# Kernel optimization log

Measured on AMD Instinct MI355X. Metric: run time of the kernel, lower is better.

Reference implementation:

```python
import jax, jax.numpy as jnp
import numpy as np

NEG_INF = -1e9  # stand-in for -inf so fully-masked rows stay finite


def setup_inputs() -> dict:
    key = jax.random.key(0)
    ks = jax.random.split(key, 7)
    B, Nq, Nkv, H, D = 8, 512, 512, 16, 256
    return {
        "v_inv": jax.random.normal(ks[0], (B, Nkv, D), dtype=jnp.float32),
        "messages": jax.random.normal(ks[1], (B, Nq, Nkv, H), dtype=jnp.float32),
        "adj_matrix": jax.random.randint(ks[2], (B, Nq, Nkv), 0, 2, dtype=jnp.int32),
        "W_in": jax.random.normal(ks[3], (D, D), dtype=jnp.float32) * (1.0 / np.sqrt(D)),
        "b_in": jax.random.normal(ks[4], (D,), dtype=jnp.float32) * 0.02,
        "W_out": jax.random.normal(ks[5], (D, D), dtype=jnp.float32) * (1.0 / np.sqrt(D)),
        "b_out": jax.random.normal(ks[6], (D,), dtype=jnp.float32) * 0.02,
    }


def reference(v_inv, messages, adj_matrix, W_in, b_in, W_out, b_out):
    H = messages.shape[-1]
    D = v_inv.shape[-1]
    d_head = D // H
    # adjacency -> additive attention mask (0 where edge, -inf where not)
    attn_mask = jnp.where(adj_matrix > 0, 0.0, NEG_INF).astype(messages.dtype)
    logits = messages + attn_mask[..., None]          # [B, Nq, Nkv, H]
    attn = jax.nn.softmax(logits, axis=2)             # softmax over N_kv
    # value projection and head split
    proj = v_inv @ W_in.T + b_in                      # [B, Nkv, D]
    head_feats = proj.reshape(*proj.shape[:-1], H, d_head)  # [B, Nkv, H, dh]
    # per-head weighted aggregation of value features
    attn_out = jnp.einsum("bqkh,bkhd->bqhd", attn, head_feats)  # [B, Nq, H, dh]
    # L2 norm of attention row per head, used as a rescale
    weights = jnp.sqrt(jnp.sum(attn * attn, axis=2))  # [B, Nq, H]
    attn_out = attn_out * weights[..., None]
    attn_out = attn_out.reshape(*attn_out.shape[:-2], D)  # [B, Nq, D]
    return attn_out @ W_out.T + b_out
```

## Files before the change

### kernel.cpp

```cpp
#include <hip/hip_runtime.h>

constexpr int NQ = 512;
constexpr int NKV = 512;
constexpr int Hh = 16;
constexpr int Dd = 256;

__global__ __launch_bounds__(256) void gemm_bias(
    const float* __restrict__ A, const float* __restrict__ W,
    const float* __restrict__ bias, float* __restrict__ C) {
  __shared__ float As[64][68];
  __shared__ float Ws[64][68];
  const int t = threadIdx.x;
  const int tx = t & 15, ty = t >> 4;
  const int m0 = blockIdx.x * 64, n0 = blockIdx.y * 64;

  float acc[4][4] = {};
  float4 av[4], wv[4];

#pragma unroll
  for (int i = 0; i < 4; ++i) {
    const int flat = i * 256 + t;
    const int r = flat >> 4, c4 = (flat & 15) << 2;
    av[i] = *(const float4*)(A + (size_t)(m0 + r) * 256 + c4);
    wv[i] = *(const float4*)(W + (size_t)(n0 + r) * 256 + c4);
  }

  for (int kb = 0; kb < 4; ++kb) {
#pragma unroll
    for (int i = 0; i < 4; ++i) {
      const int flat = i * 256 + t;
      const int r = flat >> 4, c4 = (flat & 15) << 2;
      As[c4 + 0][r] = av[i].x; As[c4 + 1][r] = av[i].y;
      As[c4 + 2][r] = av[i].z; As[c4 + 3][r] = av[i].w;
      Ws[c4 + 0][r] = wv[i].x; Ws[c4 + 1][r] = wv[i].y;
      Ws[c4 + 2][r] = wv[i].z; Ws[c4 + 3][r] = wv[i].w;
    }
    __syncthreads();
    if (kb < 3) {
#pragma unroll
      for (int i = 0; i < 4; ++i) {
        const int flat = i * 256 + t;
        const int r = flat >> 4, c4 = (flat & 15) << 2;
        av[i] = *(const float4*)(A + (size_t)(m0 + r) * 256 + (kb + 1) * 64 + c4);
        wv[i] = *(const float4*)(W + (size_t)(n0 + r) * 256 + (kb + 1) * 64 + c4);
      }
    }
#pragma unroll 16
    for (int k = 0; k < 64; ++k) {
      float a_[4], w_[4];
      *(float4*)a_ = *(const float4*)&As[k][ty << 2];
      *(float4*)w_ = *(const float4*)&Ws[k][tx << 2];
#pragma unroll
      for (int i = 0; i < 4; ++i)
#pragma unroll
        for (int j = 0; j < 4; ++j)
          acc[i][j] = fmaf(a_[i], w_[j], acc[i][j]);
    }
    if (kb < 3) __syncthreads();
  }

  const float4 bv = *(const float4*)(bias + n0 + (tx << 2));
  const float bb[4] = {bv.x, bv.y, bv.z, bv.w};
#pragma unroll
  for (int i = 0; i < 4; ++i) {
    float4 cv;
    cv.x = acc[i][0] + bb[0]; cv.y = acc[i][1] + bb[1];
    cv.z = acc[i][2] + bb[2]; cv.w = acc[i][3] + bb[3];
    *(float4*)(C + (size_t)(m0 + (ty << 2) + i) * 256 + n0 + (tx << 2)) = cv;
  }
}

__global__ __launch_bounds__(512, 4) void attn_fused(
    const float* __restrict__ msg, const int* __restrict__ adj,
    const float* __restrict__ proj, float* __restrict__ attn_out) {
  __shared__ float Psh[4][8][256];
  __shared__ float Esh[4][8][16][12];

  const int t    = threadIdx.x;
  const int lane = t & 63;
  const int w    = t >> 6;
  const int oct  = w >> 1;
  const int qh   = w & 1;
  const int h    = lane >> 2;
  const int d4   = lane & 3;
  const int col  = lane << 2;
  const int q0   = blockIdx.x * 8;
  const int b    = blockIdx.y;

  const int p_h4  = t & 3;
  const int p_q   = (t >> 2) & 7;
  const int p_oct = (t >> 5) & 3;
  const int p_jp  = t >> 7;

  const float* mrow = msg + ((size_t)(b * NQ + q0 + p_q) * NKV) * Hh + p_h4 * 4;
  const int*   arow = adj + (size_t)(b * NQ + q0 + p_q) * NKV;
  const float* pb   = proj + (size_t)b * NKV * Dd;

  float4 o[4] = {};
  float s[4] = {}, r[4] = {};

  float4 mv0, mv1;
  int a0, a1;
  {
    const int kg = p_oct * 128 + p_jp * 2;
    mv0 = *(const float4*)(mrow + (size_t)kg * Hh);
    mv1 = *(const float4*)(mrow + (size_t)(kg + 1) * Hh);
    a0 = arow[kg]; a1 = arow[kg + 1];
  }

  for (int rd = 0; rd < 16; ++rd) {
#pragma unroll
    for (int i = 0; i < 4; ++i) {
      const float* g = pb + (size_t)(i * 128 + rd * 8 + w) * Dd + (lane << 2);
      __builtin_amdgcn_global_load_lds(
          (const __attribute__((address_space(1))) unsigned int*)g,
          (__attribute__((address_space(3))) unsigned int*)&Psh[i][w][0],
          16, 0, 0);
    }
    {
      float e0[4], e1[4];
      e0[0] = a0 > 0 ? __expf(mv0.x) : 0.f; e0[1] = a0 > 0 ? __expf(mv0.y) : 0.f;
      e0[2] = a0 > 0 ? __expf(mv0.z) : 0.f; e0[3] = a0 > 0 ? __expf(mv0.w) : 0.f;
      e1[0] = a1 > 0 ? __expf(mv1.x) : 0.f; e1[1] = a1 > 0 ? __expf(mv1.y) : 0.f;
      e1[2] = a1 > 0 ? __expf(mv1.z) : 0.f; e1[3] = a1 > 0 ? __expf(mv1.w) : 0.f;
#pragma unroll
      for (int i = 0; i < 4; ++i) {
        const int h2 = (p_h4 * 4 + i) ^ p_q;
        *(float2*)&Esh[p_oct][p_q][h2][p_jp * 2] = make_float2(e0[i], e1[i]);
      }
    }
    __syncthreads();

    if (rd < 15) {
      const int kg = p_oct * 128 + (rd + 1) * 8 + p_jp * 2;
      mv0 = *(const float4*)(mrow + (size_t)kg * Hh);
      mv1 = *(const float4*)(mrow + (size_t)(kg + 1) * Hh);
      a0 = arow[kg]; a1 = arow[kg + 1];
    }

    __builtin_amdgcn_s_setprio(1);
#pragma unroll
    for (int kh = 0; kh < 2; ++kh) {
      float4 p[4];
#pragma unroll
      for (int j = 0; j < 4; ++j)
        p[j] = *(const float4*)&Psh[oct][kh * 4 + j][col];
#pragma unroll
      for (int qi = 0; qi < 4; ++qi) {
        const int ql = qh * 4 + qi;
        const float4 e4 = *(const float4*)&Esh[oct][ql][h ^ ql][kh * 4];
        s[qi] += e4.x + e4.y + e4.z + e4.w;
        r[qi] = fmaf(e4.x, e4.x, fmaf(e4.y, e4.y,
                fmaf(e4.z, e4.z, fmaf(e4.w, e4.w, r[qi]))));
        o[qi].x = fmaf(e4.x, p[0].x, o[qi].x);
        o[qi].y = fmaf(e4.x, p[0].y, o[qi].y);
        o[qi].z = fmaf(e4.x, p[0].z, o[qi].z);
        o[qi].w = fmaf(e4.x, p[0].w, o[qi].w);
        o[qi].x = fmaf(e4.y, p[1].x, o[qi].x);
        o[qi].y = fmaf(e4.y, p[1].y, o[qi].y);
        o[qi].z = fmaf(e4.y, p[1].z, o[qi].z);
        o[qi].w = fmaf(e4.y, p[1].w, o[qi].w);
        o[qi].x = fmaf(e4.z, p[2].x, o[qi].x);
        o[qi].y = fmaf(e4.z, p[2].y, o[qi].y);
        o[qi].z = fmaf(e4.z, p[2].z, o[qi].z);
        o[qi].w = fmaf(e4.z, p[2].w, o[qi].w);
        o[qi].x = fmaf(e4.w, p[3].x, o[qi].x);
        o[qi].y = fmaf(e4.w, p[3].y, o[qi].y);
        o[qi].z = fmaf(e4.w, p[3].z, o[qi].z);
        o[qi].w = fmaf(e4.w, p[3].w, o[qi].w);
      }
    }
    __builtin_amdgcn_s_setprio(0);
    if (rd < 15) __syncthreads();
  }

  float4* Ro = (float4*)&Psh[0][0][0];
  float*  Rs = &Esh[0][0][0][0];
  float*  Rr = Rs + 256;

  __syncthreads();
  if (w >= 4) {
    const int reg = w - 4;
#pragma unroll
    for (int qi = 0; qi < 4; ++qi) {
      Ro[(reg * 4 + qi) * 64 + lane] = o[qi];
      if (d4 == 0) {
        Rs[(reg * 4 + qi) * 16 + h] = s[qi];
        Rr[(reg * 4 + qi) * 16 + h] = r[qi];
      }
    }
  }
  __syncthreads();
  if (w < 4) {
#pragma unroll
    for (int qi = 0; qi < 4; ++qi) {
      const float4 v = Ro[(w * 4 + qi) * 64 + lane];
      o[qi].x += v.x; o[qi].y += v.y; o[qi].z += v.z; o[qi].w += v.w;
      s[qi] += Rs[(w * 4 + qi) * 16 + h];
      r[qi] += Rr[(w * 4 + qi) * 16 + h];
    }
  }
  __syncthreads();
  if (w == 2 || w == 3) {
    const int reg = w - 2;
#pragma unroll
    for (int qi = 0; qi < 4; ++qi) {
      Ro[(reg * 4 + qi) * 64 + lane] = o[qi];
      if (d4 == 0) {
        Rs[(reg * 4 + qi) * 16 + h] = s[qi];
        Rr[(reg * 4 + qi) * 16 + h] = r[qi];
      }
    }
  }
  __syncthreads();
  if (w < 2) {
#pragma unroll
    for (int qi = 0; qi < 4; ++qi) {
      const float4 v = Ro[(w * 4 + qi) * 64 + lane];
      o[qi].x += v.x; o[qi].y += v.y; o[qi].z += v.z; o[qi].w += v.w;
      const float st = s[qi] + Rs[(w * 4 + qi) * 16 + h];
      const float rt = r[qi] + Rr[(w * 4 + qi) * 16 + h];
      const float wgt = sqrtf(rt) / (st * st);
      float4 u;
      u.x = o[qi].x * wgt; u.y = o[qi].y * wgt;
      u.z = o[qi].z * wgt; u.w = o[qi].w * wgt;
      const int q = q0 + w * 4 + qi;
      *(float4*)(attn_out + (size_t)(b * NQ + q) * Dd + col) = u;
    }
  }
}

extern "C" void kernel_launch(void* const* d_in, const int* in_sizes, int n_in,
                              void* d_out, int out_size, void* d_ws, size_t ws_size,
                              hipStream_t stream) {
  const float* v_inv    = (const float*)d_in[0];
  const float* messages = (const float*)d_in[1];
  const int*   adj      = (const int*)d_in[2];
  const float* W_in     = (const float*)d_in[3];
  const float* b_in     = (const float*)d_in[4];
  const float* W_out    = (const float*)d_in[5];
  const float* b_out    = (const float*)d_in[6];
  float* out = (float*)d_out;

  float* proj = (float*)d_ws;
  float* attn = proj + (size_t)8 * NKV * Dd;

  dim3 gg(64, 4);
  gemm_bias<<<gg, 256, 0, stream>>>(v_inv, W_in, b_in, proj);
  attn_fused<<<dim3(64, 8), 512, 0, stream>>>(messages, adj, proj, attn);
  gemm_bias<<<gg, 256, 0, stream>>>(attn, W_out, b_out, out);
}
```

Before: 251.1 us.

## Load proj rows directly to registers and double-buffer exp tile with single barrier

Each wave now reads its eight proj rows straight from global memory into registers instead of staging them through shared memory with global_load_lds. The exp-weight tile in LDS is double-buffered, so each round needs only one barrier instead of two. The loop is unrolled by two with ping-pong message/adjacency prefetch registers, and the adjacency pair is loaded as one int2. This cuts LDS traffic and synchronisation, but adds register pressure and redundant global/L2 reads of proj, since both waves per octant now load the same rows.

```diff
diff --git a/kernel.cpp b/kernel.cpp
--- a/kernel.cpp
+++ b/kernel.cpp
@@ -73,8 +73,7 @@
 __global__ __launch_bounds__(512, 4) void attn_fused(
     const float* __restrict__ msg, const int* __restrict__ adj,
     const float* __restrict__ proj, float* __restrict__ attn_out) {
-  __shared__ float Psh[4][8][256];
-  __shared__ float Esh[4][8][16][12];
+  __shared__ float Esh[2][4][8][16][12];
 
   const int t    = threadIdx.x;
   const int lane = t & 63;
@@ -99,84 +98,90 @@
   float4 o[4] = {};
   float s[4] = {}, r[4] = {};
 
-  float4 mv0, mv1;
-  int a0, a1;
+  float4 mA0, mA1, mB0, mB1;
+  int2 aA, aB;
   {
     const int kg = p_oct * 128 + p_jp * 2;
-    mv0 = *(const float4*)(mrow + (size_t)kg * Hh);
-    mv1 = *(const float4*)(mrow + (size_t)(kg + 1) * Hh);
-    a0 = arow[kg]; a1 = arow[kg + 1];
-  }
-
-  for (int rd = 0; rd < 16; ++rd) {
-#pragma unroll
-    for (int i = 0; i < 4; ++i) {
-      const float* g = pb + (size_t)(i * 128 + rd * 8 + w) * Dd + (lane << 2);
-      __builtin_amdgcn_global_load_lds(
-          (const __attribute__((address_space(1))) unsigned int*)g,
-          (__attribute__((address_space(3))) unsigned int*)&Psh[i][w][0],
-          16, 0, 0);
-    }
-    {
-      float e0[4], e1[4];
-      e0[0] = a0 > 0 ? __expf(mv0.x) : 0.f; e0[1] = a0 > 0 ? __expf(mv0.y) : 0.f;
-      e0[2] = a0 > 0 ? __expf(mv0.z) : 0.f; e0[3] = a0 > 0 ? __expf(mv0.w) : 0.f;
-      e1[0] = a1 > 0 ? __expf(mv1.x) : 0.f; e1[1] = a1 > 0 ? __expf(mv1.y) : 0.f;
-      e1[2] = a1 > 0 ? __expf(mv1.z) : 0.f; e1[3] = a1 > 0 ? __expf(mv1.w) : 0.f;
-#pragma unroll
-      for (int i = 0; i < 4; ++i) {
-        const int h2 = (p_h4 * 4 + i) ^ p_q;
-        *(float2*)&Esh[p_oct][p_q][h2][p_jp * 2] = make_float2(e0[i], e1[i]);
-      }
-    }
-    __syncthreads();
-
-    if (rd < 15) {
-      const int kg = p_oct * 128 + (rd + 1) * 8 + p_jp * 2;
-      mv0 = *(const float4*)(mrow + (size_t)kg * Hh);
-      mv1 = *(const float4*)(mrow + (size_t)(kg + 1) * Hh);
-      a0 = arow[kg]; a1 = arow[kg + 1];
-    }
-
-    __builtin_amdgcn_s_setprio(1);
-#pragma unroll
-    for (int kh = 0; kh < 2; ++kh) {
-      float4 p[4];
-#pragma unroll
-      for (int j = 0; j < 4; ++j)
-        p[j] = *(const float4*)&Psh[oct][kh * 4 + j][col];
-#pragma unroll
-      for (int qi = 0; qi < 4; ++qi) {
-        const int ql = qh * 4 + qi;
-        const float4 e4 = *(const float4*)&Esh[oct][ql][h ^ ql][kh * 4];
-        s[qi] += e4.x + e4.y + e4.z + e4.w;
-        r[qi] = fmaf(e4.x, e4.x, fmaf(e4.y, e4.y,
-                fmaf(e4.z, e4.z, fmaf(e4.w, e4.w, r[qi]))));
-        o[qi].x = fmaf(e4.x, p[0].x, o[qi].x);
-        o[qi].y = fmaf(e4.x, p[0].y, o[qi].y);
-        o[qi].z = fmaf(e4.x, p[0].z, o[qi].z);
-        o[qi].w = fmaf(e4.x, p[0].w, o[qi].w);
-        o[qi].x = fmaf(e4.y, p[1].x, o[qi].x);
-        o[qi].y = fmaf(e4.y, p[1].y, o[qi].y);
-        o[qi].z = fmaf(e4.y, p[1].z, o[qi].z);
-        o[qi].w = fmaf(e4.y, p[1].w, o[qi].w);
-        o[qi].x = fmaf(e4.z, p[2].x, o[qi].x);
-        o[qi].y = fmaf(e4.z, p[2].y, o[qi].y);
-        o[qi].z = fmaf(e4.z, p[2].z, o[qi].z);
-        o[qi].w = fmaf(e4.z, p[2].w, o[qi].w);
-        o[qi].x = fmaf(e4.w, p[3].x, o[qi].x);
-        o[qi].y = fmaf(e4.w, p[3].y, o[qi].y);
-        o[qi].z = fmaf(e4.w, p[3].z, o[qi].z);
-        o[qi].w = fmaf(e4.w, p[3].w, o[qi].w);
-      }
-    }
-    __builtin_amdgcn_s_setprio(0);
-    if (rd < 15) __syncthreads();
-  }
-
-  float4* Ro = (float4*)&Psh[0][0][0];
-  float*  Rs = &Esh[0][0][0][0];
-  float*  Rr = Rs + 256;
+    mA0 = *(const float4*)(mrow + (size_t)kg * Hh);
+    mA1 = *(const float4*)(mrow + (size_t)(kg + 1) * Hh);
+    aA = *(const int2*)(arow + kg);
+  }
+
+#define ATTN_ROUND(RD, BUF, MC0, MC1, AC, MN0, MN1, AN)                        \
+  {                                                                            \
+     \
+     \
+    float4 p4[8];                                                              \
+    _Pragma("unroll")                                                          \
+    for (int j = 0; j < 8; ++j)                                                \
+      p4[j] = *(const float4*)(pb + (size_t)(oct * 128 + (RD) * 8 + j) * Dd + col); \
+    {                                                                          \
+      float e0[4], e1[4];                                                      \
+      e0[0] = AC.x > 0 ? __expf(MC0.x) : 0.f;                                  \
+      e0[1] = AC.x > 0 ? __expf(MC0.y) : 0.f;                                  \
+      e0[2] = AC.x > 0 ? __expf(MC0.z) : 0.f;                                  \
+      e0[3] = AC.x > 0 ? __expf(MC0.w) : 0.f;                                  \
+      e1[0] = AC.y > 0 ? __expf(MC1.x) : 0.f;                                  \
+      e1[1] = AC.y > 0 ? __expf(MC1.y) : 0.f;                                  \
+      e1[2] = AC.y > 0 ? __expf(MC1.z) : 0.f;                                  \
+      e1[3] = AC.y > 0 ? __expf(MC1.w) : 0.f;                                  \
+      _Pragma("unroll")                                                        \
+      for (int i = 0; i < 4; ++i) {                                            \
+        const int h2 = (p_h4 * 4 + i) ^ p_q;                                   \
+        *(float2*)&Esh[BUF][p_oct][p_q][h2][p_jp * 2] =                        \
+            make_float2(e0[i], e1[i]);                                         \
+      }                                                                        \
+    }                                                                          \
+    if ((RD) < 15) {  \
+      const int kg = p_oct * 128 + ((RD) + 1) * 8 + p_jp * 2;                  \
+      MN0 = *(const float4*)(mrow + (size_t)kg * Hh);                          \
+      MN1 = *(const float4*)(mrow + (size_t)(kg + 1) * Hh);                    \
+      AN = *(const int2*)(arow + kg);                                          \
+    }                                                                          \
+    asm volatile("s_waitcnt lgkmcnt(0)" ::: "memory");   \
+    __builtin_amdgcn_s_barrier();                                              \
+    __builtin_amdgcn_s_setprio(1);                                             \
+    _Pragma("unroll")                                                          \
+    for (int kh = 0; kh < 2; ++kh) {                                           \
+      _Pragma("unroll")                                                        \
+      for (int qi = 0; qi < 4; ++qi) {                                         \
+        const int ql = qh * 4 + qi;                                            \
+        const float4 e4 = *(const float4*)&Esh[BUF][oct][ql][h ^ ql][kh * 4];  \
+        s[qi] += e4.x + e4.y + e4.z + e4.w;                                    \
+        r[qi] = fmaf(e4.x, e4.x, fmaf(e4.y, e4.y,                              \
+                fmaf(e4.z, e4.z, fmaf(e4.w, e4.w, r[qi]))));                   \
+        o[qi].x = fmaf(e4.x, p4[kh * 4 + 0].x, o[qi].x);                       \
+        o[qi].y = fmaf(e4.x, p4[kh * 4 + 0].y, o[qi].y);                       \
+        o[qi].z = fmaf(e4.x, p4[kh * 4 + 0].z, o[qi].z);                       \
+        o[qi].w = fmaf(e4.x, p4[kh * 4 + 0].w, o[qi].w);                       \
+        o[qi].x = fmaf(e4.y, p4[kh * 4 + 1].x, o[qi].x);                       \
+        o[qi].y = fmaf(e4.y, p4[kh * 4 + 1].y, o[qi].y);                       \
+        o[qi].z = fmaf(e4.y, p4[kh * 4 + 1].z, o[qi].z);                       \
+        o[qi].w = fmaf(e4.y, p4[kh * 4 + 1].w, o[qi].w);                       \
+        o[qi].x = fmaf(e4.z, p4[kh * 4 + 2].x, o[qi].x);                       \
+        o[qi].y = fmaf(e4.z, p4[kh * 4 + 2].y, o[qi].y);                       \
+        o[qi].z = fmaf(e4.z, p4[kh * 4 + 2].z, o[qi].z);                       \
+        o[qi].w = fmaf(e4.z, p4[kh * 4 + 2].w, o[qi].w);                       \
+        o[qi].x = fmaf(e4.w, p4[kh * 4 + 3].x, o[qi].x);                       \
+        o[qi].y = fmaf(e4.w, p4[kh * 4 + 3].y, o[qi].y);                       \
+        o[qi].z = fmaf(e4.w, p4[kh * 4 + 3].z, o[qi].z);                       \
+        o[qi].w = fmaf(e4.w, p4[kh * 4 + 3].w, o[qi].w);                       \
+      }                                                                        \
+    }                                                                          \
+    __builtin_amdgcn_s_setprio(0);                                             \
+  }
+
+  for (int rr = 0; rr < 8; ++rr) {
+    const int rdE = rr * 2;
+    ATTN_ROUND(rdE,     0, mA0, mA1, aA, mB0, mB1, aB);
+    ATTN_ROUND(rdE + 1, 1, mB0, mB1, aB, mA0, mA1, aA);
+  }
+#undef ATTN_ROUND
+
+  float*  base = &Esh[0][0][0][0][0];
+  float4* Ro = (float4*)base;
+  float*  Rs = base + 4096;
+  float*  Rr = base + 4352;
 
   __syncthreads();
   if (w >= 4) {
```

After: 419.3 us. 67.0% more time.

## Double-buffer attention LDS stages with smaller k-chunks and one barrier per round

Applied to the files above, without the earlier changes.

Restructures the attention kernel main loop to use double-buffered shared memory for the projected values and exponentiated logits. The k-chunk per round drops from 8 to 4 keys, so there are now 32 rounds. The next chunk's global-to-LDS loads and message loads are issued before computing on the current buffer, and the exp/mask write goes to the alternate buffer after compute, leaving one barrier per round instead of two. This aims to hide global load latency behind FMA work, at the cost of more loop iterations with less compute each.

```diff
diff --git a/kernel.cpp b/kernel.cpp
--- a/kernel.cpp
+++ b/kernel.cpp
@@ -73,8 +73,8 @@
 __global__ __launch_bounds__(512, 4) void attn_fused(
     const float* __restrict__ msg, const int* __restrict__ adj,
     const float* __restrict__ proj, float* __restrict__ attn_out) {
-  __shared__ float Psh[4][8][256];
-  __shared__ float Esh[4][8][16][12];
+  __shared__ float Psh[2][4][4][256];
+  __shared__ float Esh[2][4][8][16][4];
 
   const int t    = threadIdx.x;
   const int lane = t & 63;
@@ -90,92 +90,122 @@
   const int p_h4  = t & 3;
   const int p_q   = (t >> 2) & 7;
   const int p_oct = (t >> 5) & 3;
-  const int p_jp  = t >> 7;
-
-  const float* mrow = msg + ((size_t)(b * NQ + q0 + p_q) * NKV) * Hh + p_h4 * 4;
-  const int*   arow = adj + (size_t)(b * NQ + q0 + p_q) * NKV;
-  const float* pb   = proj + (size_t)b * NKV * Dd;
+  const int p_kk  = t >> 7;
+
+  const int sa = w * 2, sb = w * 2 + 1;
+  const int sa_oct = sa >> 2, sa_kk = sa & 3;
+  const int sb_oct = sb >> 2, sb_kk = sb & 3;
+
+  const float* mrow  = msg + ((size_t)(b * NQ + q0 + p_q) * NKV) * Hh + p_h4 * 4;
+  const int*   arow  = adj + (size_t)(b * NQ + q0 + p_q) * NKV;
+  const float* pbase = proj + (size_t)b * NKV * Dd;
 
   float4 o[4] = {};
   float s[4] = {}, r[4] = {};
 
-  float4 mv0, mv1;
-  int a0, a1;
+  float4 mv; int aa;
+
   {
-    const int kg = p_oct * 128 + p_jp * 2;
-    mv0 = *(const float4*)(mrow + (size_t)kg * Hh);
-    mv1 = *(const float4*)(mrow + (size_t)(kg + 1) * Hh);
-    a0 = arow[kg]; a1 = arow[kg + 1];
-  }
-
-  for (int rd = 0; rd < 16; ++rd) {
-#pragma unroll
-    for (int i = 0; i < 4; ++i) {
-      const float* g = pb + (size_t)(i * 128 + rd * 8 + w) * Dd + (lane << 2);
+    const int kg = p_oct * 128 + p_kk;
+    mv = *(const float4*)(mrow + (size_t)kg * Hh);
+    aa = arow[kg];
+    const float* ga = pbase + (size_t)(sa_oct * 128 + sa_kk) * Dd + (lane << 2);
+    __builtin_amdgcn_global_load_lds(
+        (const __attribute__((address_space(1))) unsigned int*)ga,
+        (__attribute__((address_space(3))) unsigned int*)&Psh[0][sa_oct][sa_kk][0],
+        16, 0, 0);
+    const float* gb = pbase + (size_t)(sb_oct * 128 + sb_kk) * Dd + (lane << 2);
+    __builtin_amdgcn_global_load_lds(
+        (const __attribute__((address_space(1))) unsigned int*)gb,
+        (__attribute__((address_space(3))) unsigned int*)&Psh[0][sb_oct][sb_kk][0],
+        16, 0, 0);
+    float e[4];
+    e[0] = aa > 0 ? __expf(mv.x) : 0.f;
+    e[1] = aa > 0 ? __expf(mv.y) : 0.f;
+    e[2] = aa > 0 ? __expf(mv.z) : 0.f;
+    e[3] = aa > 0 ? __expf(mv.w) : 0.f;
+#pragma unroll
+    for (int i = 0; i < 4; ++i)
+      Esh[0][p_oct][p_q][(p_h4 * 4 + i) ^ p_q][p_kk] = e[i];
+  }
+  __syncthreads();
+
+#pragma unroll 1
+  for (int rd = 0; rd < 32; ++rd) {
+    const int cur = rd & 1, nxt = cur ^ 1;
+    if (rd < 31) {
+      const float* ga =
+          pbase + (size_t)(sa_oct * 128 + (rd + 1) * 4 + sa_kk) * Dd + (lane << 2);
       __builtin_amdgcn_global_load_lds(
-          (const __attribute__((address_space(1))) unsigned int*)g,
-          (__attribute__((address_space(3))) unsigned int*)&Psh[i][w][0],
+          (const __attribute__((address_space(1))) unsigned int*)ga,
+          (__attribute__((address_space(3))) unsigned int*)&Psh[nxt][sa_oct][sa_kk][0],
           16, 0, 0);
-    }
+      const float* gb =
+          pbase + (size_t)(sb_oct * 128 + (rd + 1) * 4 + sb_kk) * Dd + (lane << 2);
+      __builtin_amdgcn_global_load_lds(
+          (const __attribute__((address_space(1))) unsigned int*)gb,
+          (__attribute__((address_space(3))) unsigned int*)&Psh[nxt][sb_oct][sb_kk][0],
+          16, 0, 0);
+      const int kg = p_oct * 128 + (rd + 1) * 4 + p_kk;
+      mv = *(const float4*)(mrow + (size_t)kg * Hh);
+      aa = arow[kg];
+    }
+
+    __builtin_amdgcn_s_setprio(1);
     {
-      float e0[4], e1[4];
-      e0[0] = a0 > 0 ? __expf(mv0.x) : 0.f; e0[1] = a0 > 0 ? __expf(mv0.y) : 0.f;
-      e0[2] = a0 > 0 ? __expf(mv0.z) : 0.f; e0[3] = a0 > 0 ? __expf(mv0.w) : 0.f;
-      e1[0] = a1 > 0 ? __expf(mv1.x) : 0.f; e1[1] = a1 > 0 ? __expf(mv1.y) : 0.f;
-      e1[2] = a1 > 0 ? __expf(mv1.z) : 0.f; e1[3] = a1 > 0 ? __expf(mv1.w) : 0.f;
-#pragma unroll
-      for (int i = 0; i < 4; ++i) {
-        const int h2 = (p_h4 * 4 + i) ^ p_q;
-        *(float2*)&Esh[p_oct][p_q][h2][p_jp * 2] = make_float2(e0[i], e1[i]);
-      }
-    }
-    __syncthreads();
-
-    if (rd < 15) {
-      const int kg = p_oct * 128 + (rd + 1) * 8 + p_jp * 2;
-      mv0 = *(const float4*)(mrow + (size_t)kg * Hh);
-      mv1 = *(const float4*)(mrow + (size_t)(kg + 1) * Hh);
-      a0 = arow[kg]; a1 = arow[kg + 1];
-    }
-
-    __builtin_amdgcn_s_setprio(1);
-#pragma unroll
-    for (int kh = 0; kh < 2; ++kh) {
-      float4 p[4];
-#pragma unroll
-      for (int j = 0; j < 4; ++j)
-        p[j] = *(const float4*)&Psh[oct][kh * 4 + j][col];
+      const float4 p0 = *(const float4*)&Psh[cur][oct][0][col];
+      const float4 p1 = *(const float4*)&Psh[cur][oct][1][col];
 #pragma unroll
       for (int qi = 0; qi < 4; ++qi) {
         const int ql = qh * 4 + qi;
-        const float4 e4 = *(const float4*)&Esh[oct][ql][h ^ ql][kh * 4];
+        const float4 e4 = *(const float4*)&Esh[cur][oct][ql][h ^ ql][0];
         s[qi] += e4.x + e4.y + e4.z + e4.w;
         r[qi] = fmaf(e4.x, e4.x, fmaf(e4.y, e4.y,
                 fmaf(e4.z, e4.z, fmaf(e4.w, e4.w, r[qi]))));
-        o[qi].x = fmaf(e4.x, p[0].x, o[qi].x);
-        o[qi].y = fmaf(e4.x, p[0].y, o[qi].y);
-        o[qi].z = fmaf(e4.x, p[0].z, o[qi].z);
-        o[qi].w = fmaf(e4.x, p[0].w, o[qi].w);
-        o[qi].x = fmaf(e4.y, p[1].x, o[qi].x);
-        o[qi].y = fmaf(e4.y, p[1].y, o[qi].y);
-        o[qi].z = fmaf(e4.y, p[1].z, o[qi].z);
-        o[qi].w = fmaf(e4.y, p[1].w, o[qi].w);
-        o[qi].x = fmaf(e4.z, p[2].x, o[qi].x);
-        o[qi].y = fmaf(e4.z, p[2].y, o[qi].y);
-        o[qi].z = fmaf(e4.z, p[2].z, o[qi].z);
-        o[qi].w = fmaf(e4.z, p[2].w, o[qi].w);
-        o[qi].x = fmaf(e4.w, p[3].x, o[qi].x);
-        o[qi].y = fmaf(e4.w, p[3].y, o[qi].y);
-        o[qi].z = fmaf(e4.w, p[3].z, o[qi].z);
-        o[qi].w = fmaf(e4.w, p[3].w, o[qi].w);
+        o[qi].x = fmaf(e4.x, p0.x, o[qi].x);
+        o[qi].y = fmaf(e4.x, p0.y, o[qi].y);
+        o[qi].z = fmaf(e4.x, p0.z, o[qi].z);
+        o[qi].w = fmaf(e4.x, p0.w, o[qi].w);
+        o[qi].x = fmaf(e4.y, p1.x, o[qi].x);
+        o[qi].y = fmaf(e4.y, p1.y, o[qi].y);
+        o[qi].z = fmaf(e4.y, p1.z, o[qi].z);
+        o[qi].w = fmaf(e4.y, p1.w, o[qi].w);
+      }
+    }
+    {
+      const float4 p2 = *(const float4*)&Psh[cur][oct][2][col];
+      const float4 p3 = *(const float4*)&Psh[cur][oct][3][col];
+#pragma unroll
+      for (int qi = 0; qi < 4; ++qi) {
+        const int ql = qh * 4 + qi;
+        const float2 e2 = *(const float2*)&Esh[cur][oct][ql][h ^ ql][2];
+        o[qi].x = fmaf(e2.x, p2.x, o[qi].x);
+        o[qi].y = fmaf(e2.x, p2.y, o[qi].y);
+        o[qi].z = fmaf(e2.x, p2.z, o[qi].z);
+        o[qi].w = fmaf(e2.x, p2.w, o[qi].w);
+        o[qi].x = fmaf(e2.y, p3.x, o[qi].x);
+        o[qi].y = fmaf(e2.y, p3.y, o[qi].y);
+        o[qi].z = fmaf(e2.y, p3.z, o[qi].z);
+        o[qi].w = fmaf(e2.y, p3.w, o[qi].w);
       }
     }
     __builtin_amdgcn_s_setprio(0);
-    if (rd < 15) __syncthreads();
-  }
-
-  float4* Ro = (float4*)&Psh[0][0][0];
-  float*  Rs = &Esh[0][0][0][0];
+
+    if (rd < 31) {
+      float e[4];
+      e[0] = aa > 0 ? __expf(mv.x) : 0.f;
+      e[1] = aa > 0 ? __expf(mv.y) : 0.f;
+      e[2] = aa > 0 ? __expf(mv.z) : 0.f;
+      e[3] = aa > 0 ? __expf(mv.w) : 0.f;
+#pragma unroll
+      for (int i = 0; i < 4; ++i)
+        Esh[nxt][p_oct][p_q][(p_h4 * 4 + i) ^ p_q][p_kk] = e[i];
+    }
+    __syncthreads();
+  }
+
+  float4* Ro = (float4*)&Psh[0][0][0][0];
+  float*  Rs = &Esh[0][0][0][0][0];
   float*  Rr = Rs + 256;
 
   __syncthreads();
```

After: 260.9 us. +3.9%, slower.

## Halve queries per block, read proj directly from global, double-buffer exp tile

Applied to the files above, without the earlier changes.

The attention kernel now handles 4 queries per block instead of 8, doubling the grid to 128x8 blocks. The shared-memory staging of proj via global_load_lds is dropped; each thread reads proj rows straight from global (L2/cache) as float4. The exp/mask tile is double-buffered so only one barrier per round remains, with 16 keys per round over 8 rounds. This trades less shared memory and fewer barriers for more global proj reads (proj reuse across queries is halved) and more blocks.

```diff
diff --git a/kernel.cpp b/kernel.cpp
--- a/kernel.cpp
+++ b/kernel.cpp
@@ -70,11 +70,10 @@
   }
 }
 
-__global__ __launch_bounds__(512, 4) void attn_fused(
+__global__ __launch_bounds__(512) void attn_fused(
     const float* __restrict__ msg, const int* __restrict__ adj,
     const float* __restrict__ proj, float* __restrict__ attn_out) {
-  __shared__ float Psh[4][8][256];
-  __shared__ float Esh[4][8][16][12];
+  __shared__ float Esh[2][4][4][16][20];
 
   const int t    = threadIdx.x;
   const int lane = t & 63;
@@ -84,149 +83,157 @@
   const int h    = lane >> 2;
   const int d4   = lane & 3;
   const int col  = lane << 2;
-  const int q0   = blockIdx.x * 8;
+  const int q0   = blockIdx.x * 4;
   const int b    = blockIdx.y;
 
   const int p_h4  = t & 3;
-  const int p_q   = (t >> 2) & 7;
-  const int p_oct = (t >> 5) & 3;
-  const int p_jp  = t >> 7;
-
-  const float* mrow = msg + ((size_t)(b * NQ + q0 + p_q) * NKV) * Hh + p_h4 * 4;
-  const int*   arow = adj + (size_t)(b * NQ + q0 + p_q) * NKV;
-  const float* pb   = proj + (size_t)b * NKV * Dd;
-
-  float4 o[4] = {};
-  float s[4] = {}, r[4] = {};
+  const int p_q   = (t >> 2) & 3;
+  const int p_oct = (t >> 4) & 3;
+  const int p_kp  = t >> 6;
+
+  const float* mrow  = msg + ((size_t)(b * NQ + q0 + p_q) * NKV) * Hh + p_h4 * 4;
+  const int*   arow  = adj + (size_t)(b * NQ + q0 + p_q) * NKV;
+  const float* pbase = proj + (size_t)b * NKV * Dd;
+
+  float4 o0 = {}, o1 = {};
+  float s0 = 0.f, s1 = 0.f, r0 = 0.f, r1 = 0.f;
 
   float4 mv0, mv1;
-  int a0, a1;
+  int2 aa;
+
+  const int ql0 = qh * 2, ql1 = qh * 2 + 1;
+  const int eh0 = h ^ ql0, eh1 = h ^ ql1;
+
   {
-    const int kg = p_oct * 128 + p_jp * 2;
+    const int kg = p_oct * 128 + p_kp * 2;
     mv0 = *(const float4*)(mrow + (size_t)kg * Hh);
     mv1 = *(const float4*)(mrow + (size_t)(kg + 1) * Hh);
-    a0 = arow[kg]; a1 = arow[kg + 1];
-  }
-
-  for (int rd = 0; rd < 16; ++rd) {
+    aa = *(const int2*)(arow + kg);
+    float e0[4], e1[4];
+    e0[0] = aa.x > 0 ? __expf(mv0.x) : 0.f; e0[1] = aa.x > 0 ? __expf(mv0.y) : 0.f;
+    e0[2] = aa.x > 0 ? __expf(mv0.z) : 0.f; e0[3] = aa.x > 0 ? __expf(mv0.w) : 0.f;
+    e1[0] = aa.y > 0 ? __expf(mv1.x) : 0.f; e1[1] = aa.y > 0 ? __expf(mv1.y) : 0.f;
+    e1[2] = aa.y > 0 ? __expf(mv1.z) : 0.f; e1[3] = aa.y > 0 ? __expf(mv1.w) : 0.f;
 #pragma unroll
     for (int i = 0; i < 4; ++i) {
-      const float* g = pb + (size_t)(i * 128 + rd * 8 + w) * Dd + (lane << 2);
-      __builtin_amdgcn_global_load_lds(
-          (const __attribute__((address_space(1))) unsigned int*)g,
-          (__attribute__((address_space(3))) unsigned int*)&Psh[i][w][0],
-          16, 0, 0);
-    }
-    {
+      const int h2 = (p_h4 * 4 + i) ^ p_q;
+      *(float2*)&Esh[0][p_oct][p_q][h2][p_kp * 2] = make_float2(e0[i], e1[i]);
+    }
+  }
+  __syncthreads();
+
+#pragma unroll 1
+  for (int rd = 0; rd < 8; ++rd) {
+    const int cur = rd & 1, nxt = cur ^ 1;
+    if (rd < 7) {
+      const int kg = p_oct * 128 + (rd + 1) * 16 + p_kp * 2;
+      mv0 = *(const float4*)(mrow + (size_t)kg * Hh);
+      mv1 = *(const float4*)(mrow + (size_t)(kg + 1) * Hh);
+      aa = *(const int2*)(arow + kg);
+    }
+
+    __builtin_amdgcn_s_setprio(1);
+#pragma unroll 1
+    for (int kq = 0; kq < 4; ++kq) {
+      const float* prow =
+          pbase + (size_t)(oct * 128 + rd * 16 + kq * 4) * Dd + col;
+      const float4 p0 = *(const float4*)(prow);
+      const float4 p1 = *(const float4*)(prow + Dd);
+      const float4 p2 = *(const float4*)(prow + 2 * Dd);
+      const float4 p3 = *(const float4*)(prow + 3 * Dd);
+      const float4 ea = *(const float4*)&Esh[cur][oct][ql0][eh0][kq * 4];
+      const float4 eb = *(const float4*)&Esh[cur][oct][ql1][eh1][kq * 4];
+      s0 += ea.x + ea.y + ea.z + ea.w;
+      r0 = fmaf(ea.x, ea.x, fmaf(ea.y, ea.y,
+           fmaf(ea.z, ea.z, fmaf(ea.w, ea.w, r0))));
+      o0.x = fmaf(ea.x, p0.x, o0.x); o0.y = fmaf(ea.x, p0.y, o0.y);
+      o0.z = fmaf(ea.x, p0.z, o0.z); o0.w = fmaf(ea.x, p0.w, o0.w);
+      o0.x = fmaf(ea.y, p1.x, o0.x); o0.y = fmaf(ea.y, p1.y, o0.y);
+      o0.z = fmaf(ea.y, p1.z, o0.z); o0.w = fmaf(ea.y, p1.w, o0.w);
+      o0.x = fmaf(ea.z, p2.x, o0.x); o0.y = fmaf(ea.z, p2.y, o0.y);
+      o0.z = fmaf(ea.z, p2.z, o0.z); o0.w = fmaf(ea.z, p2.w, o0.w);
+      o0.x = fmaf(ea.w, p3.x, o0.x); o0.y = fmaf(ea.w, p3.y, o0.y);
+      o0.z = fmaf(ea.w, p3.z, o0.z); o0.w = fmaf(ea.w, p3.w, o0.w);
+      s1 += eb.x + eb.y + eb.z + eb.w;
+      r1 = fmaf(eb.x, eb.x, fmaf(eb.y, eb.y,
+           fmaf(eb.z, eb.z, fmaf(eb.w, eb.w, r1))));
+      o1.x = fmaf(eb.x, p0.x, o1.x); o1.y = fmaf(eb.x, p0.y, o1.y);
+      o1.z = fmaf(eb.x, p0.z, o1.z); o1.w = fmaf(eb.x, p0.w, o1.w);
+      o1.x = fmaf(eb.y, p1.x, o1.x); o1.y = fmaf(eb.y, p1.y, o1.y);
+      o1.z = fmaf(eb.y, p1.z, o1.z); o1.w = fmaf(eb.y, p1.w, o1.w);
+      o1.x = fmaf(eb.z, p2.x, o1.x); o1.y = fmaf(eb.z, p2.y, o1.y);
+      o1.z = fmaf(eb.z, p2.z, o1.z); o1.w = fmaf(eb.z, p2.w, o1.w);
+      o1.x = fmaf(eb.w, p3.x, o1.x); o1.y = fmaf(eb.w, p3.y, o1.y);
+      o1.z = fmaf(eb.w, p3.z, o1.z); o1.w = fmaf(eb.w, p3.w, o1.w);
+    }
+    __builtin_amdgcn_s_setprio(0);
+
+    if (rd < 7) {
       float e0[4], e1[4];
-      e0[0] = a0 > 0 ? __expf(mv0.x) : 0.f; e0[1] = a0 > 0 ? __expf(mv0.y) : 0.f;
-      e0[2] = a0 > 0 ? __expf(mv0.z) : 0.f; e0[3] = a0 > 0 ? __expf(mv0.w) : 0.f;
-      e1[0] = a1 > 0 ? __expf(mv1.x) : 0.f; e1[1] = a1 > 0 ? __expf(mv1.y) : 0.f;
-      e1[2] = a1 > 0 ? __expf(mv1.z) : 0.f; e1[3] = a1 > 0 ? __expf(mv1.w) : 0.f;
+      e0[0] = aa.x > 0 ? __expf(mv0.x) : 0.f; e0[1] = aa.x > 0 ? __expf(mv0.y) : 0.f;
+      e0[2] = aa.x > 0 ? __expf(mv0.z) : 0.f; e0[3] = aa.x > 0 ? __expf(mv0.w) : 0.f;
+      e1[0] = aa.y > 0 ? __expf(mv1.x) : 0.f; e1[1] = aa.y > 0 ? __expf(mv1.y) : 0.f;
+      e1[2] = aa.y > 0 ? __expf(mv1.z) : 0.f; e1[3] = aa.y > 0 ? __expf(mv1.w) : 0.f;
 #pragma unroll
       for (int i = 0; i < 4; ++i) {
         const int h2 = (p_h4 * 4 + i) ^ p_q;
-        *(float2*)&Esh[p_oct][p_q][h2][p_jp * 2] = make_float2(e0[i], e1[i]);
+        *(float2*)&Esh[nxt][p_oct][p_q][h2][p_kp * 2] = make_float2(e0[i], e1[i]);
       }
     }
     __syncthreads();
-
-    if (rd < 15) {
-      const int kg = p_oct * 128 + (rd + 1) * 8 + p_jp * 2;
-      mv0 = *(const float4*)(mrow + (size_t)kg * Hh);
-      mv1 = *(const float4*)(mrow + (size_t)(kg + 1) * Hh);
-      a0 = arow[kg]; a1 = arow[kg + 1];
-    }
-
-    __builtin_amdgcn_s_setprio(1);
-#pragma unroll
-    for (int kh = 0; kh < 2; ++kh) {
-      float4 p[4];
-#pragma unroll
-      for (int j = 0; j < 4; ++j)
-        p[j] = *(const float4*)&Psh[oct][kh * 4 + j][col];
-#pragma unroll
-      for (int qi = 0; qi < 4; ++qi) {
-        const int ql = qh * 4 + qi;
-        const float4 e4 = *(const float4*)&Esh[oct][ql][h ^ ql][kh * 4];
-        s[qi] += e4.x + e4.y + e4.z + e4.w;
-        r[qi] = fmaf(e4.x, e4.x, fmaf(e4.y, e4.y,
-                fmaf(e4.z, e4.z, fmaf(e4.w, e4.w, r[qi]))));
-        o[qi].x = fmaf(e4.x, p[0].x, o[qi].x);
-        o[qi].y = fmaf(e4.x, p[0].y, o[qi].y);
-        o[qi].z = fmaf(e4.x, p[0].z, o[qi].z);
-        o[qi].w = fmaf(e4.x, p[0].w, o[qi].w);
-        o[qi].x = fmaf(e4.y, p[1].x, o[qi].x);
-        o[qi].y = fmaf(e4.y, p[1].y, o[qi].y);
-        o[qi].z = fmaf(e4.y, p[1].z, o[qi].z);
-        o[qi].w = fmaf(e4.y, p[1].w, o[qi].w);
-        o[qi].x = fmaf(e4.z, p[2].x, o[qi].x);
-        o[qi].y = fmaf(e4.z, p[2].y, o[qi].y);
-        o[qi].z = fmaf(e4.z, p[2].z, o[qi].z);
-        o[qi].w = fmaf(e4.z, p[2].w, o[qi].w);
-        o[qi].x = fmaf(e4.w, p[3].x, o[qi].x);
-        o[qi].y = fmaf(e4.w, p[3].y, o[qi].y);
-        o[qi].z = fmaf(e4.w, p[3].z, o[qi].z);
-        o[qi].w = fmaf(e4.w, p[3].w, o[qi].w);
-      }
-    }
-    __builtin_amdgcn_s_setprio(0);
-    if (rd < 15) __syncthreads();
-  }
-
-  float4* Ro = (float4*)&Psh[0][0][0];
-  float*  Rs = &Esh[0][0][0][0];
-  float*  Rr = Rs + 256;
+  }
+
+  float* base = &Esh[0][0][0][0][0];
+  float4* Ro = (float4*)base;
+  float*  Rs = base + 2048;
+  float*  Rr = base + 2176;
 
   __syncthreads();
   if (w >= 4) {
     const int reg = w - 4;
-#pragma unroll
-    for (int qi = 0; qi < 4; ++qi) {
-      Ro[(reg * 4 + qi) * 64 + lane] = o[qi];
-      if (d4 == 0) {
-        Rs[(reg * 4 + qi) * 16 + h] = s[qi];
-        Rr[(reg * 4 + qi) * 16 + h] = r[qi];
-      }
+    Ro[(reg * 2 + 0) * 64 + lane] = o0;
+    Ro[(reg * 2 + 1) * 64 + lane] = o1;
+    if (d4 == 0) {
+      Rs[(reg * 2 + 0) * 16 + h] = s0; Rs[(reg * 2 + 1) * 16 + h] = s1;
+      Rr[(reg * 2 + 0) * 16 + h] = r0; Rr[(reg * 2 + 1) * 16 + h] = r1;
     }
   }
   __syncthreads();
   if (w < 4) {
-#pragma unroll
-    for (int qi = 0; qi < 4; ++qi) {
-      const float4 v = Ro[(w * 4 + qi) * 64 + lane];
-      o[qi].x += v.x; o[qi].y += v.y; o[qi].z += v.z; o[qi].w += v.w;
-      s[qi] += Rs[(w * 4 + qi) * 16 + h];
-      r[qi] += Rr[(w * 4 + qi) * 16 + h];
-    }
+    const float4 v0 = Ro[(w * 2 + 0) * 64 + lane];
+    const float4 v1 = Ro[(w * 2 + 1) * 64 + lane];
+    o0.x += v0.x; o0.y += v0.y; o0.z += v0.z; o0.w += v0.w;
+    o1.x += v1.x; o1.y += v1.y; o1.z += v1.z; o1.w += v1.w;
+    s0 += Rs[(w * 2 + 0) * 16 + h]; s1 += Rs[(w * 2 + 1) * 16 + h];
+    r0 += Rr[(w * 2 + 0) * 16 + h]; r1 += Rr[(w * 2 + 1) * 16 + h];
   }
   __syncthreads();
   if (w == 2 || w == 3) {
     const int reg = w - 2;
-#pragma unroll
-    for (int qi = 0; qi < 4; ++qi) {
-      Ro[(reg * 4 + qi) * 64 + lane] = o[qi];
-      if (d4 == 0) {
-        Rs[(reg * 4 + qi) * 16 + h] = s[qi];
-        Rr[(reg * 4 + qi) * 16 + h] = r[qi];
-      }
+    Ro[(reg * 2 + 0) * 64 + lane] = o0;
+    Ro[(reg * 2 + 1) * 64 + lane] = o1;
+    if (d4 == 0) {
+      Rs[(reg * 2 + 0) * 16 + h] = s0; Rs[(reg * 2 + 1) * 16 + h] = s1;
+      Rr[(reg * 2 + 0) * 16 + h] = r0; Rr[(reg * 2 + 1) * 16 + h] = r1;
     }
   }
   __syncthreads();
   if (w < 2) {
-#pragma unroll
-    for (int qi = 0; qi < 4; ++qi) {
-      const float4 v = Ro[(w * 4 + qi) * 64 + lane];
-      o[qi].x += v.x; o[qi].y += v.y; o[qi].z += v.z; o[qi].w += v.w;
-      const float st = s[qi] + Rs[(w * 4 + qi) * 16 + h];
-      const float rt = r[qi] + Rr[(w * 4 + qi) * 16 + h];
-      const float wgt = sqrtf(rt) / (st * st);
-      float4 u;
-      u.x = o[qi].x * wgt; u.y = o[qi].y * wgt;
-      u.z = o[qi].z * wgt; u.w = o[qi].w * wgt;
-      const int q = q0 + w * 4 + qi;
-      *(float4*)(attn_out + (size_t)(b * NQ + q) * Dd + col) = u;
-    }
+    const float4 v0 = Ro[(w * 2 + 0) * 64 + lane];
+    const float4 v1 = Ro[(w * 2 + 1) * 64 + lane];
+    o0.x += v0.x; o0.y += v0.y; o0.z += v0.z; o0.w += v0.w;
+    o1.x += v1.x; o1.y += v1.y; o1.z += v1.z; o1.w += v1.w;
+    const float st0 = s0 + Rs[(w * 2 + 0) * 16 + h];
+    const float st1 = s1 + Rs[(w * 2 + 1) * 16 + h];
+    const float rt0 = r0 + Rr[(w * 2 + 0) * 16 + h];
+    const float rt1 = r1 + Rr[(w * 2 + 1) * 16 + h];
+    const float wg0 = sqrtf(rt0) / (st0 * st0);
+    const float wg1 = sqrtf(rt1) / (st1 * st1);
+    float4 u0, u1;
+    u0.x = o0.x * wg0; u0.y = o0.y * wg0; u0.z = o0.z * wg0; u0.w = o0.w * wg0;
+    u1.x = o1.x * wg1; u1.y = o1.y * wg1; u1.z = o1.z * wg1; u1.w = o1.w * wg1;
+    *(float4*)(attn_out + (size_t)(b * NQ + q0 + w * 2 + 0) * Dd + col) = u0;
+    *(float4*)(attn_out + (size_t)(b * NQ + q0 + w * 2 + 1) * Dd + col) = u1;
   }
 }
 
@@ -247,6 +254,6 @@
 
   dim3 gg(64, 4);
   gemm_bias<<<gg, 256, 0, stream>>>(v_inv, W_in, b_in, proj);
-  attn_fused<<<dim3(64, 8), 512, 0, stream>>>(messages, adj, proj, attn);
+  attn_fused<<<dim3(128, 8), 512, 0, stream>>>(messages, adj, proj, attn);
   gemm_bias<<<gg, 256, 0, stream>>>(attn, W_out, b_out, out);
 }
```

Result: slower. 266.5 us (+6.1%).
